# Kernel tuning notes

Measured on AMD Instinct MI355X. Metric: run time of the kernel, lower is better.

The kernel has to match this reference:

```python
import jax, jax.numpy as jnp
import numpy as np

IN_FEATURES = 4096
OUT_FEATURES = 4096
NUM_GROUPS = 16
GROUP_IN = IN_FEATURES // NUM_GROUPS    # 256
GROUP_OUT = OUT_FEATURES // NUM_GROUPS  # 256
BATCH = 8192


def setup_inputs() -> dict:
    key = jax.random.key(0)
    kx, kw, kb = jax.random.split(key, 3)
    x = jax.random.normal(kx, (BATCH, IN_FEATURES), dtype=jnp.float32)
    # nn.Linear weight is [out, in]; stack per-group -> [G, dout_g, din_g]
    bound = 1.0 / np.sqrt(GROUP_IN)
    W = jax.random.uniform(kw, (NUM_GROUPS, GROUP_OUT, GROUP_IN), dtype=jnp.float32,
                           minval=-bound, maxval=bound)
    b = jax.random.uniform(kb, (NUM_GROUPS, GROUP_OUT), dtype=jnp.float32,
                           minval=-bound, maxval=bound)
    return {"x": x, "W": W, "b": b}


def reference(x, W, b):
    B = x.shape[0]
    # split along features -> [B, G, din_g]; block-diagonal matmul as batched GEMM
    xg = x.reshape(B, NUM_GROUPS, GROUP_IN)
    # y[b,g,o] = sum_i xg[b,g,i] * W[g,o,i] + b[g,o]
    yg = jnp.einsum('bgi,goi->bgo', xg, W) + b
    return yg.reshape(B, OUT_FEATURES)
```

## Files before the change

kernel.cpp:

```cpp
#include <hip/hip_runtime.h>
#include <hip/hip_bf16.h>
#include <stdint.h>


#define IN_F   4096
#define OUT_F  4096
#define GIN    256
#define GOUT   256

#define BM 128
#define BN 128
#define BK 64
#define KTOT 256

using short8  = __attribute__((ext_vector_type(8))) short;
using floatx4 = __attribute__((ext_vector_type(4))) float;

__device__ __forceinline__ short f2bf_rne(float f) {
    unsigned u = __builtin_bit_cast(unsigned, f);
    unsigned r = u + 0x7FFFu + ((u >> 16) & 1u);
    return (short)(r >> 16);
}

__global__ __launch_bounds__(256, 2)
void grouped_linear_kernel(const float* __restrict__ X,
                           const float* __restrict__ W,
                           const float* __restrict__ Bias,
                           float* __restrict__ Out) {
    __shared__ __align__(16) short lsA[BM * BK];
    __shared__ __align__(16) short lsB[BN * BK];

    const int t    = threadIdx.x;
    const int lane = t & 63;
    const int wave = t >> 6;
    const int wm   = wave >> 1;
    const int wn   = wave & 1;
    const int lrow = lane & 15;
    const int quad = lane >> 4;

    const int bn   = blockIdx.x & 31;
    const int bm   = blockIdx.x >> 5;
    const int g    = bn >> 1;
    const int row0 = bm * BM;
    const int col0 = bn * BN;
    const int nlb  = (bn & 1) * BN;

    const float* Wg = W + (size_t)g * GOUT * GIN + (size_t)nlb * GIN;
    const float* Xg = X + (size_t)row0 * IN_F + g * GIN;

    floatx4 acc[4][4];
    #pragma unroll
    for (int i = 0; i < 4; ++i)
        #pragma unroll
        for (int j = 0; j < 4; ++j)
            acc[i][j] = (floatx4){0.f, 0.f, 0.f, 0.f};

    const int c8 = (t & 7) * 8;
    const int q0 = (t & 7);

    for (int kt = 0; kt < KTOT / BK; ++kt) {
        const int kbase = kt * BK;

        #pragma unroll
        for (int i = 0; i < 4; ++i) {
            int r = (t >> 3) + 32 * i;
            const float* src = Xg + (size_t)r * IN_F + kbase + c8;
            floatx4 f0 = *(const floatx4*)src;
            floatx4 f1 = *(const floatx4*)(src + 4);
            short8 p;
            p[0] = f2bf_rne(f0[0]); p[1] = f2bf_rne(f0[1]);
            p[2] = f2bf_rne(f0[2]); p[3] = f2bf_rne(f0[3]);
            p[4] = f2bf_rne(f1[0]); p[5] = f2bf_rne(f1[1]);
            p[6] = f2bf_rne(f1[2]); p[7] = f2bf_rne(f1[3]);
            int q = q0 ^ (r & 7);
            *(short8*)&lsA[r * BK + q * 8] = p;
        }
        #pragma unroll
        for (int i = 0; i < 4; ++i) {
            int n = (t >> 3) + 32 * i;
            const float* src = Wg + (size_t)n * GIN + kbase + c8;
            floatx4 f0 = *(const floatx4*)src;
            floatx4 f1 = *(const floatx4*)(src + 4);
            short8 p;
            p[0] = f2bf_rne(f0[0]); p[1] = f2bf_rne(f0[1]);
            p[2] = f2bf_rne(f0[2]); p[3] = f2bf_rne(f0[3]);
            p[4] = f2bf_rne(f1[0]); p[5] = f2bf_rne(f1[1]);
            p[6] = f2bf_rne(f1[2]); p[7] = f2bf_rne(f1[3]);
            int q = q0 ^ (n & 7);
            *(short8*)&lsB[n * BK + q * 8] = p;
        }
        __syncthreads();

        #pragma unroll
        for (int kk = 0; kk < 2; ++kk) {
            int kb = kk * 32 + quad * 8;
            int qs = kb >> 3;
            short8 a[4], b[4];
            #pragma unroll
            for (int i = 0; i < 4; ++i) {
                int r = wm * 64 + i * 16 + lrow;
                a[i] = *(const short8*)&lsA[r * BK + ((qs ^ (r & 7)) * 8)];
            }
            #pragma unroll
            for (int j = 0; j < 4; ++j) {
                int n = wn * 64 + j * 16 + lrow;
                b[j] = *(const short8*)&lsB[n * BK + ((qs ^ (n & 7)) * 8)];
            }
            #pragma unroll
            for (int i = 0; i < 4; ++i)
                #pragma unroll
                for (int j = 0; j < 4; ++j)
                    acc[i][j] = __builtin_amdgcn_mfma_f32_16x16x32_bf16(
                        a[i], b[j], acc[i][j], 0, 0, 0);
        }
        __syncthreads();
    }

    #pragma unroll
    for (int j = 0; j < 4; ++j) {
        int gc = col0 + wn * 64 + j * 16 + lrow;
        float bias = Bias[gc];
        #pragma unroll
        for (int i = 0; i < 4; ++i) {
            int gr = row0 + wm * 64 + i * 16 + quad * 4;
            floatx4 v = acc[i][j];
            #pragma unroll
            for (int rg = 0; rg < 4; ++rg)
                Out[(size_t)(gr + rg) * OUT_F + gc] = v[rg] + bias;
        }
    }
}

extern "C" void kernel_launch(void* const* d_in, const int* in_sizes, int n_in,
                              void* d_out, int out_size, void* d_ws, size_t ws_size,
                              hipStream_t stream) {
    const float* X    = (const float*)d_in[0];
    const float* W    = (const float*)d_in[1];
    const float* Bias = (const float*)d_in[2];
    float*       Out  = (float*)d_out;

    dim3 grid(64 * 32);
    dim3 block(256);
    grouped_linear_kernel<<<grid, block, 0, stream>>>(X, W, Bias, Out);
}
```

Before: 272.2 us.

## Drop LDS staging and load MFMA fragments directly from global memory

Removes the shared-memory tiles and barriers. Each wave now loads its A and B fragments straight from global memory into registers, converts them to bf16, and feeds them to the MFMAs over a fully unrolled K loop. The block index is also swizzled so that co-resident blocks share groups and rows, which should improve L2 reuse. This avoids LDS write/read traffic and the syncs, but each wave re-fetches data that its sibling waves also need. The per-lane accesses are only 32 bytes contiguous per row, so global load efficiency may drop and register pressure rises.

New measurement: 333.6 us. +22.5%, slower.

```diff
diff --git a/kernel.cpp b/kernel.cpp
--- a/kernel.cpp
+++ b/kernel.cpp
@@ -8,11 +8,6 @@
 #define GIN    256
 #define GOUT   256
 
-#define BM 128
-#define BN 128
-#define BK 64
-#define KTOT 256
-
 using short8  = __attribute__((ext_vector_type(8))) short;
 using floatx4 = __attribute__((ext_vector_type(4))) float;
 
@@ -22,14 +17,20 @@
     return (short)(r >> 16);
 }
 
+__device__ __forceinline__ short8 pack8(floatx4 f0, floatx4 f1) {
+    short8 p;
+    p[0] = f2bf_rne(f0[0]); p[1] = f2bf_rne(f0[1]);
+    p[2] = f2bf_rne(f0[2]); p[3] = f2bf_rne(f0[3]);
+    p[4] = f2bf_rne(f1[0]); p[5] = f2bf_rne(f1[1]);
+    p[6] = f2bf_rne(f1[2]); p[7] = f2bf_rne(f1[3]);
+    return p;
+}
+
 __global__ __launch_bounds__(256, 2)
 void grouped_linear_kernel(const float* __restrict__ X,
                            const float* __restrict__ W,
                            const float* __restrict__ Bias,
                            float* __restrict__ Out) {
-    __shared__ __align__(16) short lsA[BM * BK];
-    __shared__ __align__(16) short lsB[BN * BK];
-
     const int t    = threadIdx.x;
     const int lane = t & 63;
     const int wave = t >> 6;
@@ -37,16 +38,24 @@
     const int wn   = wave & 1;
     const int lrow = lane & 15;
     const int quad = lane >> 4;
+    const int koff = quad * 8;
 
-    const int bn   = blockIdx.x & 31;
-    const int bm   = blockIdx.x >> 5;
-    const int g    = bn >> 1;
-    const int row0 = bm * BM;
-    const int col0 = bn * BN;
-    const int nlb  = (bn & 1) * BN;
+    const int bid = blockIdx.x;
+    const int swz = (bid & 7) * 256 + (bid >> 3);
+    const int bn  = swz & 31;
+    const int bm  = swz >> 5;
+    const int g   = bn >> 1;
+    const int row0 = bm * 128 + wm * 64;
+    const int coln = (bn & 1) * 128 + wn * 64;
 
-    const float* Wg = W + (size_t)g * GOUT * GIN + (size_t)nlb * GIN;
-    const float* Xg = X + (size_t)row0 * IN_F + g * GIN;
+    const float* pa[4];
+    const float* pb[4];
+    #pragma unroll
+    for (int i = 0; i < 4; ++i)
+        pa[i] = X + (size_t)(row0 + i * 16 + lrow) * IN_F + g * GIN + koff;
+    #pragma unroll
+    for (int j = 0; j < 4; ++j)
+        pb[j] = W + (size_t)g * GOUT * GIN + (size_t)(coln + j * 16 + lrow) * GIN + koff;
 
     floatx4 acc[4][4];
     #pragma unroll
@@ -55,78 +64,42 @@
         for (int j = 0; j < 4; ++j)
             acc[i][j] = (floatx4){0.f, 0.f, 0.f, 0.f};
 
-    const int c8 = (t & 7) * 8;
-    const int q0 = (t & 7);
-
-    for (int kt = 0; kt < KTOT / BK; ++kt) {
-        const int kbase = kt * BK;
-
+    #pragma unroll
+    for (int ks = 0; ks < 8; ++ks) {
+        short8 a[4], b[4];
         #pragma unroll
         for (int i = 0; i < 4; ++i) {
-            int r = (t >> 3) + 32 * i;
-            const float* src = Xg + (size_t)r * IN_F + kbase + c8;
-            floatx4 f0 = *(const floatx4*)src;
-            floatx4 f1 = *(const floatx4*)(src + 4);
-            short8 p;
-            p[0] = f2bf_rne(f0[0]); p[1] = f2bf_rne(f0[1]);
-            p[2] = f2bf_rne(f0[2]); p[3] = f2bf_rne(f0[3]);
-            p[4] = f2bf_rne(f1[0]); p[5] = f2bf_rne(f1[1]);
-            p[6] = f2bf_rne(f1[2]); p[7] = f2bf_rne(f1[3]);
-            int q = q0 ^ (r & 7);
-            *(short8*)&lsA[r * BK + q * 8] = p;
+            floatx4 f0 = *(const floatx4*)(pa[i] + ks * 32);
+            floatx4 f1 = *(const floatx4*)(pa[i] + ks * 32 + 4);
+            a[i] = pack8(f0, f1);
         }
         #pragma unroll
-        for (int i = 0; i < 4; ++i) {
-            int n = (t >> 3) + 32 * i;
-            const float* src = Wg + (size_t)n * GIN + kbase + c8;
-            floatx4 f0 = *(const floatx4*)src;
-            floatx4 f1 = *(const floatx4*)(src + 4);
-            short8 p;
-            p[0] = f2bf_rne(f0[0]); p[1] = f2bf_rne(f0[1]);
-            p[2] = f2bf_rne(f0[2]); p[3] = f2bf_rne(f0[3]);
-            p[4] = f2bf_rne(f1[0]); p[5] = f2bf_rne(f1[1]);
-            p[6] = f2bf_rne(f1[2]); p[7] = f2bf_rne(f1[3]);
-            int q = q0 ^ (n & 7);
-            *(short8*)&lsB[n * BK + q * 8] = p;
+        for (int j = 0; j < 4; ++j) {
+            floatx4 f0 = *(const floatx4*)(pb[j] + ks * 32);
+            floatx4 f1 = *(const floatx4*)(pb[j] + ks * 32 + 4);
+            b[j] = pack8(f0, f1);
         }
-        __syncthreads();
-
         #pragma unroll
-        for (int kk = 0; kk < 2; ++kk) {
-            int kb = kk * 32 + quad * 8;
-            int qs = kb >> 3;
-            short8 a[4], b[4];
+        for (int i = 0; i < 4; ++i)
             #pragma unroll
-            for (int i = 0; i < 4; ++i) {
-                int r = wm * 64 + i * 16 + lrow;
-                a[i] = *(const short8*)&lsA[r * BK + ((qs ^ (r & 7)) * 8)];
-            }
-            #pragma unroll
-            for (int j = 0; j < 4; ++j) {
-                int n = wn * 64 + j * 16 + lrow;
-                b[j] = *(const short8*)&lsB[n * BK + ((qs ^ (n & 7)) * 8)];
-            }
-            #pragma unroll
-            for (int i = 0; i < 4; ++i)
-                #pragma unroll
-                for (int j = 0; j < 4; ++j)
-                    acc[i][j] = __builtin_amdgcn_mfma_f32_16x16x32_bf16(
-                        a[i], b[j], acc[i][j], 0, 0, 0);
-        }
-        __syncthreads();
+            for (int j = 0; j < 4; ++j)
+                acc[i][j] = __builtin_amdgcn_mfma_f32_16x16x32_bf16(
+                    a[i], b[j], acc[i][j], 0, 0, 0);
     }
 
+    float bias[4];
     #pragma unroll
-    for (int j = 0; j < 4; ++j) {
-        int gc = col0 + wn * 64 + j * 16 + lrow;
-        float bias = Bias[gc];
+    for (int j = 0; j < 4; ++j)
+        bias[j] = Bias[g * GOUT + coln + j * 16 + lrow];
+
+    #pragma unroll
+    for (int i = 0; i < 4; ++i) {
         #pragma unroll
-        for (int i = 0; i < 4; ++i) {
-            int gr = row0 + wm * 64 + i * 16 + quad * 4;
-            floatx4 v = acc[i][j];
+        for (int rg = 0; rg < 4; ++rg) {
+            size_t rowoff = (size_t)(row0 + i * 16 + quad * 4 + rg) * OUT_F;
             #pragma unroll
-            for (int rg = 0; rg < 4; ++rg)
-                Out[(size_t)(gr + rg) * OUT_F + gc] = v[rg] + bias;
+            for (int j = 0; j < 4; ++j)
+                Out[rowoff + g * GOUT + coln + j * 16 + lrow] = acc[i][j][rg] + bias[j];
         }
     }
 }
```

## Double-buffer LDS tiles and prefetch next K-tile into registers

Applied to the files above, without the earlier changes.

Splits the K loop into load, convert-and-write, and compute phases over two shared-memory buffers. The global loads for the next tile are issued before the current tile is computed, so load latency can hide behind the MFMA work, and each step needs one barrier instead of two. In exchange it doubles LDS use to 64KB per block and holds 64 extra prefetch registers per thread, which may reduce occupancy. The custom barrier waits only on lgkmcnt.

Measured after the change: 257.1 us. 1.06x faster.

```diff
diff --git a/kernel.cpp b/kernel.cpp
--- a/kernel.cpp
+++ b/kernel.cpp
@@ -1,5 +1,4 @@
 #include <hip/hip_runtime.h>
-#include <hip/hip_bf16.h>
 #include <stdint.h>
 
 
@@ -22,13 +21,29 @@
     return (short)(r >> 16);
 }
 
+__device__ __forceinline__ short8 pack8(floatx4 f0, floatx4 f1) {
+    short8 p;
+    p[0] = f2bf_rne(f0[0]); p[1] = f2bf_rne(f0[1]);
+    p[2] = f2bf_rne(f0[2]); p[3] = f2bf_rne(f0[3]);
+    p[4] = f2bf_rne(f1[0]); p[5] = f2bf_rne(f1[1]);
+    p[6] = f2bf_rne(f1[2]); p[7] = f2bf_rne(f1[3]);
+    return p;
+}
+
+#define SYNC_PHASE() do {                                        \
+    asm volatile("s_waitcnt lgkmcnt(0)" ::: "memory");           \
+    __builtin_amdgcn_sched_barrier(0);                           \
+    __builtin_amdgcn_s_barrier();                                \
+    __builtin_amdgcn_sched_barrier(0);                           \
+} while (0)
+
 __global__ __launch_bounds__(256, 2)
 void grouped_linear_kernel(const float* __restrict__ X,
                            const float* __restrict__ W,
                            const float* __restrict__ Bias,
                            float* __restrict__ Out) {
-    __shared__ __align__(16) short lsA[BM * BK];
-    __shared__ __align__(16) short lsB[BN * BK];
+    __shared__ __align__(16) short lsA[2][BM * BK];
+    __shared__ __align__(16) short lsB[2][BN * BK];
 
     const int t    = threadIdx.x;
     const int lane = t & 63;
@@ -57,40 +72,42 @@
 
     const int c8 = (t & 7) * 8;
     const int q0 = (t & 7);
+    const int r0 = (t >> 3);
 
-    for (int kt = 0; kt < KTOT / BK; ++kt) {
+    floatx4 ra[4][2], rb[4][2];
+
+    auto LOADS = [&](int kt) {
         const int kbase = kt * BK;
-
         #pragma unroll
         for (int i = 0; i < 4; ++i) {
-            int r = (t >> 3) + 32 * i;
-            const float* src = Xg + (size_t)r * IN_F + kbase + c8;
-            floatx4 f0 = *(const floatx4*)src;
-            floatx4 f1 = *(const floatx4*)(src + 4);
-            short8 p;
-            p[0] = f2bf_rne(f0[0]); p[1] = f2bf_rne(f0[1]);
-            p[2] = f2bf_rne(f0[2]); p[3] = f2bf_rne(f0[3]);
-            p[4] = f2bf_rne(f1[0]); p[5] = f2bf_rne(f1[1]);
-            p[6] = f2bf_rne(f1[2]); p[7] = f2bf_rne(f1[3]);
-            int q = q0 ^ (r & 7);
-            *(short8*)&lsA[r * BK + q * 8] = p;
+            const float* src = Xg + (size_t)(r0 + 32 * i) * IN_F + kbase + c8;
+            ra[i][0] = *(const floatx4*)src;
+            ra[i][1] = *(const floatx4*)(src + 4);
         }
         #pragma unroll
         for (int i = 0; i < 4; ++i) {
-            int n = (t >> 3) + 32 * i;
-            const float* src = Wg + (size_t)n * GIN + kbase + c8;
-            floatx4 f0 = *(const floatx4*)src;
-            floatx4 f1 = *(const floatx4*)(src + 4);
-            short8 p;
-            p[0] = f2bf_rne(f0[0]); p[1] = f2bf_rne(f0[1]);
-            p[2] = f2bf_rne(f0[2]); p[3] = f2bf_rne(f0[3]);
-            p[4] = f2bf_rne(f1[0]); p[5] = f2bf_rne(f1[1]);
-            p[6] = f2bf_rne(f1[2]); p[7] = f2bf_rne(f1[3]);
+            const float* src = Wg + (size_t)(r0 + 32 * i) * GIN + kbase + c8;
+            rb[i][0] = *(const floatx4*)src;
+            rb[i][1] = *(const floatx4*)(src + 4);
+        }
+    };
+
+    auto WRITE = [&](int buf) {
+        #pragma unroll
+        for (int i = 0; i < 4; ++i) {
+            int r = r0 + 32 * i;
+            int q = q0 ^ (r & 7);
+            *(short8*)&lsA[buf][r * BK + q * 8] = pack8(ra[i][0], ra[i][1]);
+        }
+        #pragma unroll
+        for (int i = 0; i < 4; ++i) {
+            int n = r0 + 32 * i;
             int q = q0 ^ (n & 7);
-            *(short8*)&lsB[n * BK + q * 8] = p;
+            *(short8*)&lsB[buf][n * BK + q * 8] = pack8(rb[i][0], rb[i][1]);
         }
-        __syncthreads();
+    };
 
+    auto COMPUTE = [&](int buf) {
         #pragma unroll
         for (int kk = 0; kk < 2; ++kk) {
             int kb = kk * 32 + quad * 8;
@@ -99,12 +116,12 @@
             #pragma unroll
             for (int i = 0; i < 4; ++i) {
                 int r = wm * 64 + i * 16 + lrow;
-                a[i] = *(const short8*)&lsA[r * BK + ((qs ^ (r & 7)) * 8)];
+                a[i] = *(const short8*)&lsA[buf][r * BK + ((qs ^ (r & 7)) * 8)];
             }
             #pragma unroll
             for (int j = 0; j < 4; ++j) {
                 int n = wn * 64 + j * 16 + lrow;
-                b[j] = *(const short8*)&lsB[n * BK + ((qs ^ (n & 7)) * 8)];
+                b[j] = *(const short8*)&lsB[buf][n * BK + ((qs ^ (n & 7)) * 8)];
             }
             #pragma unroll
             for (int i = 0; i < 4; ++i)
@@ -113,8 +130,24 @@
                     acc[i][j] = __builtin_amdgcn_mfma_f32_16x16x32_bf16(
                         a[i], b[j], acc[i][j], 0, 0, 0);
         }
-        __syncthreads();
-    }
+    };
+
+    LOADS(0);
+    WRITE(0);
+    LOADS(1);
+    SYNC_PHASE();
+    COMPUTE(0);
+    WRITE(1);
+    LOADS(2);
+    SYNC_PHASE();
+    COMPUTE(1);
+    WRITE(0);
+    LOADS(3);
+    SYNC_PHASE();
+    COMPUTE(0);
+    WRITE(1);
+    SYNC_PHASE();
+    COMPUTE(1);
 
     #pragma unroll
     for (int j = 0; j < 4; ++j) {
```

## Shrink tiles to 64x64, raise occupancy, swizzle block order, use lighter barriers

Applied to the files above, without the earlier changes.

Tile size drops from 128x128 to 64x64, so the grid grows fourfold and each wave holds a 2x2 MFMA accumulator instead of 4x4. A waves_per_eu hint of 6 targets higher occupancy to hide global-load latency. Block IDs are swizzled so consecutive blocks share column tiles for L2 reuse. __syncthreads is replaced by an explicit lgkmcnt wait plus s_barrier with sched_barriers. The cost is lower arithmetic intensity: every X element is now loaded and converted four times per group instead of twice, which adds global traffic on a memory-bound shape.

Measured after the change: 279.2 us. +2.6%, slower.

```diff
diff --git a/kernel.cpp b/kernel.cpp
--- a/kernel.cpp
+++ b/kernel.cpp
@@ -1,5 +1,4 @@
 #include <hip/hip_runtime.h>
-#include <hip/hip_bf16.h>
 #include <stdint.h>
 
 
@@ -8,8 +7,8 @@
 #define GIN    256
 #define GOUT   256
 
-#define BM 128
-#define BN 128
+#define BM 64
+#define BN 64
 #define BK 64
 #define KTOT 256
 
@@ -22,7 +21,23 @@
     return (short)(r >> 16);
 }
 
-__global__ __launch_bounds__(256, 2)
+__device__ __forceinline__ short8 pack8(floatx4 f0, floatx4 f1) {
+    short8 p;
+    p[0] = f2bf_rne(f0[0]); p[1] = f2bf_rne(f0[1]);
+    p[2] = f2bf_rne(f0[2]); p[3] = f2bf_rne(f0[3]);
+    p[4] = f2bf_rne(f1[0]); p[5] = f2bf_rne(f1[1]);
+    p[6] = f2bf_rne(f1[2]); p[7] = f2bf_rne(f1[3]);
+    return p;
+}
+
+#define SYNC_PHASE() do {                                        \
+    asm volatile("s_waitcnt lgkmcnt(0)" ::: "memory");           \
+    __builtin_amdgcn_sched_barrier(0);                           \
+    __builtin_amdgcn_s_barrier();                                \
+    __builtin_amdgcn_sched_barrier(0);                           \
+} while (0)
+
+__global__ __launch_bounds__(256) __attribute__((amdgpu_waves_per_eu(6)))
 void grouped_linear_kernel(const float* __restrict__ X,
                            const float* __restrict__ W,
                            const float* __restrict__ Bias,
@@ -38,91 +53,83 @@
     const int lrow = lane & 15;
     const int quad = lane >> 4;
 
-    const int bn   = blockIdx.x & 31;
-    const int bm   = blockIdx.x >> 5;
-    const int g    = bn >> 1;
+    const int bid = blockIdx.x;
+    const int swz = (bid & 7) * 1024 + (bid >> 3);
+    const int bn  = swz >> 7;
+    const int bm  = swz & 127;
+    const int g   = bn >> 2;
     const int row0 = bm * BM;
     const int col0 = bn * BN;
-    const int nlb  = (bn & 1) * BN;
+    const int nlb  = (bn & 3) * BN;
 
     const float* Wg = W + (size_t)g * GOUT * GIN + (size_t)nlb * GIN;
     const float* Xg = X + (size_t)row0 * IN_F + g * GIN;
 
-    floatx4 acc[4][4];
+    floatx4 acc[2][2];
     #pragma unroll
-    for (int i = 0; i < 4; ++i)
+    for (int i = 0; i < 2; ++i)
         #pragma unroll
-        for (int j = 0; j < 4; ++j)
+        for (int j = 0; j < 2; ++j)
             acc[i][j] = (floatx4){0.f, 0.f, 0.f, 0.f};
 
     const int c8 = (t & 7) * 8;
     const int q0 = (t & 7);
+    const int r0 = (t >> 3);
 
     for (int kt = 0; kt < KTOT / BK; ++kt) {
         const int kbase = kt * BK;
 
         #pragma unroll
-        for (int i = 0; i < 4; ++i) {
-            int r = (t >> 3) + 32 * i;
+        for (int it = 0; it < 2; ++it) {
+            int r = r0 + 32 * it;
             const float* src = Xg + (size_t)r * IN_F + kbase + c8;
             floatx4 f0 = *(const floatx4*)src;
             floatx4 f1 = *(const floatx4*)(src + 4);
-            short8 p;
-            p[0] = f2bf_rne(f0[0]); p[1] = f2bf_rne(f0[1]);
-            p[2] = f2bf_rne(f0[2]); p[3] = f2bf_rne(f0[3]);
-            p[4] = f2bf_rne(f1[0]); p[5] = f2bf_rne(f1[1]);
-            p[6] = f2bf_rne(f1[2]); p[7] = f2bf_rne(f1[3]);
             int q = q0 ^ (r & 7);
-            *(short8*)&lsA[r * BK + q * 8] = p;
+            *(short8*)&lsA[r * BK + q * 8] = pack8(f0, f1);
         }
         #pragma unroll
-        for (int i = 0; i < 4; ++i) {
-            int n = (t >> 3) + 32 * i;
+        for (int it = 0; it < 2; ++it) {
+            int n = r0 + 32 * it;
             const float* src = Wg + (size_t)n * GIN + kbase + c8;
             floatx4 f0 = *(const floatx4*)src;
             floatx4 f1 = *(const floatx4*)(src + 4);
-            short8 p;
-            p[0] = f2bf_rne(f0[0]); p[1] = f2bf_rne(f0[1]);
-            p[2] = f2bf_rne(f0[2]); p[3] = f2bf_rne(f0[3]);
-            p[4] = f2bf_rne(f1[0]); p[5] = f2bf_rne(f1[1]);
-            p[6] = f2bf_rne(f1[2]); p[7] = f2bf_rne(f1[3]);
             int q = q0 ^ (n & 7);
-            *(short8*)&lsB[n * BK + q * 8] = p;
+            *(short8*)&lsB[n * BK + q * 8] = pack8(f0, f1);
         }
-        __syncthreads();
+        SYNC_PHASE();
 
         #pragma unroll
         for (int kk = 0; kk < 2; ++kk) {
-            int kb = kk * 32 + quad * 8;
-            int qs = kb >> 3;
-            short8 a[4], b[4];
+            int qs = kk * 4 + quad;
+            short8 a[2], b[2];
             #pragma unroll
-            for (int i = 0; i < 4; ++i) {
-                int r = wm * 64 + i * 16 + lrow;
+            for (int i = 0; i < 2; ++i) {
+                int r = wm * 32 + i * 16 + lrow;
                 a[i] = *(const short8*)&lsA[r * BK + ((qs ^ (r & 7)) * 8)];
             }
             #pragma unroll
-            for (int j = 0; j < 4; ++j) {
-                int n = wn * 64 + j * 16 + lrow;
+            for (int j = 0; j < 2; ++j) {
+                int n = wn * 32 + j * 16 + lrow;
                 b[j] = *(const short8*)&lsB[n * BK + ((qs ^ (n & 7)) * 8)];
             }
             #pragma unroll
-            for (int i = 0; i < 4; ++i)
+            for (int i = 0; i < 2; ++i)
                 #pragma unroll
-                for (int j = 0; j < 4; ++j)
+                for (int j = 0; j < 2; ++j)
                     acc[i][j] = __builtin_amdgcn_mfma_f32_16x16x32_bf16(
                         a[i], b[j], acc[i][j], 0, 0, 0);
         }
-        __syncthreads();
+        SYNC_PHASE();
     }
 
     #pragma unroll
-    for (int j = 0; j < 4; ++j) {
-        int gc = col0 + wn * 64 + j * 16 + lrow;
+    for (int j = 0; j < 2; ++j) {
+        int gc = col0 + wn * 32 + j * 16 + lrow;
         float bias = Bias[gc];
         #pragma unroll
-        for (int i = 0; i < 4; ++i) {
-            int gr = row0 + wm * 64 + i * 16 + quad * 4;
+        for (int i = 0; i < 2; ++i) {
+            int gr = row0 + wm * 32 + i * 16 + quad * 4;
             floatx4 v = acc[i][j];
             #pragma unroll
             for (int rg = 0; rg < 4; ++rg)
@@ -139,7 +146,7 @@
     const float* Bias = (const float*)d_in[2];
     float*       Out  = (float*)d_out;
 
-    dim3 grid(64 * 32);
+    dim3 grid(128 * 64);
     dim3 block(256);
     grouped_linear_kernel<<<grid, block, 0, stream>>>(X, W, Bias, Out);
 }
```
